# Kernel optimization log

Hardware: AMD Instinct MI355X
Metric: run time of the kernel (lower is better)

Reference implementation:

```python
import jax, jax.numpy as jnp
import numpy as np

F = 16      # frames
NV = 4096   # visual points per frame
NT = 512    # tactile points per frame
M = 4096    # model points
SCALE = 0.1


def setup_inputs() -> dict:
    key = jax.random.key(0)
    ks = jax.random.split(key, 6)
    return {
        "state": jax.random.normal(ks[0], (6,), dtype=jnp.float32) * 0.1,
        "model_points": jax.random.normal(ks[1], (M, 3), dtype=jnp.float32),
        "visual_points": jax.random.normal(ks[2], (F, NV, 3), dtype=jnp.float32),
        "tactile_points": jax.random.normal(ks[3], (F, NT, 3), dtype=jnp.float32),
        "physics_pred_states": jax.random.normal(ks[4], (F, 12), dtype=jnp.float32) * 0.1,
        "delta_time": jax.random.uniform(ks[5], (F,), dtype=jnp.float32, minval=0.01, maxval=0.05),
    }


def _skew(a):
    z = jnp.zeros((), a.dtype)
    return jnp.array([[z, -a[2], a[1]],
                      [a[2], z, -a[0]],
                      [-a[1], a[0], z]])


def _rot_from_omega(omega, dt):
    # Rodrigues: R = I + sin(theta*dt) S + (1 - cos(theta*dt)) S@S, S = skew(omega/|omega|)
    theta = jnp.linalg.norm(omega)
    ax = omega / jnp.clip(theta, 1e-8)
    S = _skew(ax)
    return jnp.eye(3, dtype=omega.dtype) + jnp.sin(theta * dt) * S + (1.0 - jnp.cos(theta * dt)) * (S @ S)


def _chamfer(pred, gt):
    # rows: pred [N,3], cols: gt [M,3]; row-min of squared distances, then mean
    d = (jnp.sum(pred * pred, axis=1)[:, None]
         + jnp.sum(gt * gt, axis=1)[None, :]
         - 2.0 * pred @ gt.T)
    return jnp.mean(jnp.min(d, axis=1))


def reference(state, model_points, visual_points, tactile_points, physics_pred_states, delta_time):
    t0 = state[:3]
    r0 = _rot_from_omega(state[3:], jnp.float32(1.0))  # Euler2Mat modeled as axis-angle

    def pose_step(carry, x):
        t, r = carry
        v, omega, dt = x
        t = t + v * dt
        r = _rot_from_omega(omega, dt) @ r
        return (t, r), (t, r)

    _, (ts, rs) = jax.lax.scan(
        pose_step, (t0, r0),
        (physics_pred_states[1:, 6:9], physics_pred_states[1:, 9:12], delta_time[1:]))
    ts = jnp.concatenate([t0[None], ts], axis=0)  # [F,3]
    rs = jnp.concatenate([r0[None], rs], axis=0)  # [F,3,3]

    def frame_loss(acc, x):
        t, r, vp, tp = x
        vc = ((vp - t) @ r) / SCALE
        tc = ((tp - t) @ r) / SCALE
        acc = acc + _chamfer(vc, model_points) + 0.1 * _chamfer(tc, model_points)
        return acc, None

    E_cd, _ = jax.lax.scan(frame_loss, jnp.zeros((), jnp.float32),
                           (ts, rs, visual_points, tactile_points))
    return E_cd
```

## Files before the change

### kernel.cpp

```cpp
#include <hip/hip_runtime.h>
#include <math.h>

#define F_    16
#define NV_   4096
#define NT_   512
#define M_    4096
#define PPF_  (NV_ + NT_)
#define NPTS_ (F_ * PPF_)
#define SCALE_INV 10.0f

#define TPB   256
#define PTSB  72
#define NBLK  (NPTS_ / PTSB)
#define NG    64
#define MPG   (M_ / NG)
#define CHM   16
#define NCH   (MPG / CHM)
#define FG    68
#define PPL   18
#define NPR   9

typedef float v2f __attribute__((ext_vector_type(2)));

__device__ inline void rot_from_omega(float ox, float oy, float oz, float dt,
                                      float* R) {
    float theta = sqrtf(ox * ox + oy * oy + oz * oz);
    float inv = 1.0f / fmaxf(theta, 1e-8f);
    float ax = ox * inv, ay = oy * inv, az = oz * inv;
    float s = sinf(theta * dt);
    float c = 1.0f - cosf(theta * dt);
    R[0] = 1.0f - c * (ay * ay + az * az);
    R[1] = -s * az + c * ax * ay;
    R[2] =  s * ay + c * ax * az;
    R[3] =  s * az + c * ax * ay;
    R[4] = 1.0f - c * (ax * ax + az * az);
    R[5] = -s * ax + c * ay * az;
    R[6] = -s * ay + c * ax * az;
    R[7] =  s * ax + c * ay * az;
    R[8] = 1.0f - c * (ax * ax + ay * ay);
}

__device__ __forceinline__ void dist6(v2f qa01, v2f qa23, v2f qb01, v2f qb23,
                                      v2f c0a, v2f c0b, v2f c0c,
                                      v2f c1a, v2f c1b, v2f c1c,
                                      v2f c2a, v2f c2b, v2f c2c, float* dmp) {
    v2f A0, A1, A2, B0, B1, B2;
    asm("v_pk_fma_f32 %0, %7, %16, %7 op_sel:[0,0,1] op_sel_hi:[0,1,1]\n\t"
        "v_pk_fma_f32 %1, %7, %17, %7 op_sel:[0,0,1] op_sel_hi:[0,1,1]\n\t"
        "v_pk_fma_f32 %2, %7, %18, %7 op_sel:[0,0,1] op_sel_hi:[0,1,1]\n\t"
        "v_pk_fma_f32 %3, %9, %16, %9 op_sel:[0,0,1] op_sel_hi:[0,1,1]\n\t"
        "v_pk_fma_f32 %4, %9, %17, %9 op_sel:[0,0,1] op_sel_hi:[0,1,1]\n\t"
        "v_pk_fma_f32 %5, %9, %18, %9 op_sel:[0,0,1] op_sel_hi:[0,1,1]\n\t"
        "v_pk_fma_f32 %0, %6, %13, %0 op_sel:[1,0,0] op_sel_hi:[1,1,1]\n\t"
        "v_pk_fma_f32 %1, %6, %14, %1 op_sel:[1,0,0] op_sel_hi:[1,1,1]\n\t"
        "v_pk_fma_f32 %2, %6, %15, %2 op_sel:[1,0,0] op_sel_hi:[1,1,1]\n\t"
        "v_pk_fma_f32 %3, %8, %13, %3 op_sel:[1,0,0] op_sel_hi:[1,1,1]\n\t"
        "v_pk_fma_f32 %4, %8, %14, %4 op_sel:[1,0,0] op_sel_hi:[1,1,1]\n\t"
        "v_pk_fma_f32 %5, %8, %15, %5 op_sel:[1,0,0] op_sel_hi:[1,1,1]\n\t"
        "v_pk_fma_f32 %0, %6, %10, %0 op_sel:[0,0,0] op_sel_hi:[0,1,1]\n\t"
        "v_pk_fma_f32 %1, %6, %11, %1 op_sel:[0,0,0] op_sel_hi:[0,1,1]\n\t"
        "v_pk_fma_f32 %2, %6, %12, %2 op_sel:[0,0,0] op_sel_hi:[0,1,1]\n\t"
        "v_pk_fma_f32 %3, %8, %10, %3 op_sel:[0,0,0] op_sel_hi:[0,1,1]\n\t"
        "v_pk_fma_f32 %4, %8, %11, %4 op_sel:[0,0,0] op_sel_hi:[0,1,1]\n\t"
        "v_pk_fma_f32 %5, %8, %12, %5 op_sel:[0,0,0] op_sel_hi:[0,1,1]"
        : "=&v"(A0), "=&v"(A1), "=&v"(A2), "=&v"(B0), "=&v"(B1), "=&v"(B2)
        : "v"(qa01), "v"(qa23), "v"(qb01), "v"(qb23),
          "v"(c0a), "v"(c0b), "v"(c0c),
          "v"(c1a), "v"(c1b), "v"(c1c),
          "v"(c2a), "v"(c2b), "v"(c2c));
    dmp[0] = fminf(fminf(A0.x, B0.x), dmp[0]);
    dmp[1] = fminf(fminf(A0.y, B0.y), dmp[1]);
    dmp[2] = fminf(fminf(A1.x, B1.x), dmp[2]);
    dmp[3] = fminf(fminf(A1.y, B1.y), dmp[3]);
    dmp[4] = fminf(fminf(A2.x, B2.x), dmp[4]);
    dmp[5] = fminf(fminf(A2.y, B2.y), dmp[5]);
}

__global__ void prep_kernel(const float* __restrict__ state,
                            const float* __restrict__ phys,
                            const float* __restrict__ dts,
                            const float* __restrict__ model,
                            float* __restrict__ ws_pose,
                            float4* __restrict__ ws_feat) {
    const int b = blockIdx.x, t = threadIdx.x;
    if (b == 0) {
        __shared__ float sRs[F_ * 9];
        __shared__ float sdt[F_ * 3];
        if (t < F_) {
            float ox, oy, oz, dt;
            if (t == 0) { ox = state[3]; oy = state[4]; oz = state[5]; dt = 1.0f; }
            else        { ox = phys[t * 12 + 9]; oy = phys[t * 12 + 10];
                          oz = phys[t * 12 + 11]; dt = dts[t]; }
            float Rs[9];
            rot_from_omega(ox, oy, oz, dt, Rs);
            for (int j = 0; j < 9; ++j) sRs[t * 9 + j] = Rs[j];
            if (t > 0) {
                sdt[t * 3 + 0] = phys[t * 12 + 6] * dt;
                sdt[t * 3 + 1] = phys[t * 12 + 7] * dt;
                sdt[t * 3 + 2] = phys[t * 12 + 8] * dt;
            }
        }
        if (t == 0) {
            float R[9];
            for (int j = 0; j < 9; ++j) R[j] = sRs[j];
            float tr[3] = {state[0], state[1], state[2]};
            for (int i = 0; i < F_; ++i) {
                if (i > 0) {
                    tr[0] += sdt[i * 3 + 0];
                    tr[1] += sdt[i * 3 + 1];
                    tr[2] += sdt[i * 3 + 2];
                    float Rn[9];
                    const float* Rsp = sRs + i * 9;
                    for (int r = 0; r < 3; ++r)
                        for (int c2 = 0; c2 < 3; ++c2)
                            Rn[r * 3 + c2] = Rsp[r * 3 + 0] * R[0 + c2] +
                                             Rsp[r * 3 + 1] * R[3 + c2] +
                                             Rsp[r * 3 + 2] * R[6 + c2];
                    for (int j = 0; j < 9; ++j) R[j] = Rn[j];
                }
                float* o = ws_pose + i * 12;
                o[0] = tr[0]; o[1] = tr[1]; o[2] = tr[2];
                for (int j = 0; j < 9; ++j) o[3 + j] = R[j] * SCALE_INV;
            }
        }
    } else {
        const int id = (b - 1) * 256 + t;
        float gx = model[id * 3 + 0], gy = model[id * 3 + 1], gz = model[id * 3 + 2];
        const int c = (id >> 4) & 3, g = id >> 6, m = id & 15;
        ws_feat[c * 1024 + g * 16 + m] =
            make_float4(-2.0f * gx, -2.0f * gy, -2.0f * gz,
                        gx * gx + gy * gy + gz * gz);
    }
}

__global__ __launch_bounds__(TPB, 4) void chamfer_main(
    const float* __restrict__ vis, const float* __restrict__ tac,
    const float* __restrict__ ws_pose, const float4* __restrict__ ws_feat,
    float* __restrict__ out) {
    __shared__ float4 feat[CHM * FG];
    __shared__ float  sdm2[NG * 80];
    __shared__ float  spose[F_ * 12];
    __shared__ float  sw[4];

    const int t  = threadIdx.x;
    const int g  = t >> 2;
    const int pl = t & 3;
    const int f  = blockIdx.x >> 6;
    const int lbase = (blockIdx.x & 63) * PTSB;

    if (t < F_ * 12) spose[t] = ws_pose[t];
#pragma unroll
    for (int j = 0; j < 4; ++j) {
        int flat = t + 256 * j;
        feat[(flat & 15) * FG + (flat >> 4)] = ws_feat[flat];
    }
    __syncthreads();

    float Rr[9], trx, try_, trz;
    {
        const float* ps = spose + f * 12;
        trx = ps[0]; try_ = ps[1]; trz = ps[2];
        for (int j = 0; j < 9; ++j) Rr[j] = ps[3 + j];
    }

    v2f c0p[NPR], c1p[NPR], c2p[NPR];
    float cn[PPL], dm[PPL];
#pragma unroll
    for (int k = 0; k < PPL; ++k) {
        int loc = lbase + pl * PPL + k;
        const float* p = (loc < NV_) ? (vis + ((size_t)f * NV_ + loc) * 3)
                                     : (tac + ((size_t)f * NT_ + (loc - NV_)) * 3);
        float d0 = p[0] - trx, d1 = p[1] - try_, d2 = p[2] - trz;
        float x = d0 * Rr[0] + d1 * Rr[3] + d2 * Rr[6];
        float y = d0 * Rr[1] + d1 * Rr[4] + d2 * Rr[7];
        float z = d0 * Rr[2] + d1 * Rr[5] + d2 * Rr[8];
        cn[k] = x * x + y * y + z * z;
        dm[k] = 3.4e38f;
        if (k & 1) { c0p[k >> 1].y = x; c1p[k >> 1].y = y; c2p[k >> 1].y = z; }
        else       { c0p[k >> 1].x = x; c1p[k >> 1].x = y; c2p[k >> 1].x = z; }
    }

    for (int c = 0;; ++c) {
#pragma unroll 2
        for (int m = 0; m < CHM; m += 2) {
            float4 ga = feat[m * FG + g];
            float4 gb = feat[(m + 1) * FG + g];
            v2f qa01 = (v2f){ga.x, ga.y}, qa23 = (v2f){ga.z, ga.w};
            v2f qb01 = (v2f){gb.x, gb.y}, qb23 = (v2f){gb.z, gb.w};
            dist6(qa01, qa23, qb01, qb23, c0p[0], c0p[1], c0p[2],
                  c1p[0], c1p[1], c1p[2], c2p[0], c2p[1], c2p[2], dm);
            dist6(qa01, qa23, qb01, qb23, c0p[3], c0p[4], c0p[5],
                  c1p[3], c1p[4], c1p[5], c2p[3], c2p[4], c2p[5], dm + 6);
            dist6(qa01, qa23, qb01, qb23, c0p[6], c0p[7], c0p[8],
                  c1p[6], c1p[7], c1p[8], c2p[6], c2p[7], c2p[8], dm + 12);
        }
        if (c == NCH - 1) break;
        __syncthreads();
#pragma unroll
        for (int j = 0; j < 4; ++j) {
            int flat = t + 256 * j;
            feat[(flat & 15) * FG + (flat >> 4)] = ws_feat[(c + 1) * 1024 + flat];
        }
        __syncthreads();
    }

    {
        float* seg = &sdm2[g * 80 + pl * 20];
#pragma unroll
        for (int k = 0; k < PPL; ++k) seg[k] = dm[k] + cn[k];
    }
    __syncthreads();

    float v = 0.0f;
    if (t < PTSB) {
        const int off = t + 2 * (t / 18);
        float mn = sdm2[off];
#pragma unroll 8
        for (int i = 1; i < NG; ++i) mn = fminf(mn, sdm2[i * 80 + off]);
        const int loc = lbase + t;
        const float w = (loc < NV_) ? (1.0f / NV_) : (0.1f / NT_);
        v = mn * w;
    }
#pragma unroll
    for (int off2 = 32; off2 > 0; off2 >>= 1) v += __shfl_down(v, off2);
    if ((t & 63) == 0) sw[t >> 6] = v;
    __syncthreads();
    if (t == 0) atomicAdd(out, sw[0] + sw[1] + sw[2] + sw[3]);
}

__global__ __launch_bounds__(TPB) void chamfer_fb(
    const float* __restrict__ state, const float* __restrict__ model,
    const float* __restrict__ vis, const float* __restrict__ tac,
    const float* __restrict__ phys, const float* __restrict__ dts,
    float* __restrict__ out) {
    __shared__ float sw[4];
    const int pt = blockIdx.x * TPB + threadIdx.x;
    const int f = pt / PPF_, loc = pt - f * PPF_;
    float R[9], tr[3] = {state[0], state[1], state[2]};
    rot_from_omega(state[3], state[4], state[5], 1.0f, R);
    for (int i = 1; i <= f; ++i) {
        float dt = dts[i];
        tr[0] += phys[i * 12 + 6] * dt;
        tr[1] += phys[i * 12 + 7] * dt;
        tr[2] += phys[i * 12 + 8] * dt;
        float Rs[9], Rn[9];
        rot_from_omega(phys[i * 12 + 9], phys[i * 12 + 10], phys[i * 12 + 11], dt, Rs);
        for (int r = 0; r < 3; ++r)
            for (int c2 = 0; c2 < 3; ++c2)
                Rn[r * 3 + c2] = Rs[r * 3 + 0] * R[0 + c2] +
                                 Rs[r * 3 + 1] * R[3 + c2] +
                                 Rs[r * 3 + 2] * R[6 + c2];
        for (int j = 0; j < 9; ++j) R[j] = Rn[j];
    }
    for (int j = 0; j < 9; ++j) R[j] *= SCALE_INV;
    const float* p = (loc < NV_) ? (vis + ((size_t)f * NV_ + loc) * 3)
                                 : (tac + ((size_t)f * NT_ + (loc - NV_)) * 3);
    float d0 = p[0] - tr[0], d1 = p[1] - tr[1], d2 = p[2] - tr[2];
    float x = d0 * R[0] + d1 * R[3] + d2 * R[6];
    float y = d0 * R[1] + d1 * R[4] + d2 * R[7];
    float z = d0 * R[2] + d1 * R[5] + d2 * R[8];
    float cn = x * x + y * y + z * z;
    float mn = 3.4e38f;
    for (int i = 0; i < M_; ++i) {
        float gx = model[i * 3], gy = model[i * 3 + 1], gz = model[i * 3 + 2];
        float gn = gx * gx + gy * gy + gz * gz;
        float dd = fmaf(-2.0f * gx, x, fmaf(-2.0f * gy, y, fmaf(-2.0f * gz, z, gn)));
        mn = fminf(mn, dd);
    }
    float w = (loc < NV_) ? (1.0f / NV_) : (0.1f / NT_);
    float v = (mn + cn) * w;
    for (int off = 32; off > 0; off >>= 1) v += __shfl_down(v, off);
    if ((threadIdx.x & 63) == 0) sw[threadIdx.x >> 6] = v;
    __syncthreads();
    if (threadIdx.x == 0) atomicAdd(out, sw[0] + sw[1] + sw[2] + sw[3]);
}

extern "C" void kernel_launch(void* const* d_in, const int* in_sizes, int n_in,
                              void* d_out, int out_size, void* d_ws, size_t ws_size,
                              hipStream_t stream) {
    const float* state = (const float*)d_in[0];
    const float* model = (const float*)d_in[1];
    const float* vis   = (const float*)d_in[2];
    const float* tac   = (const float*)d_in[3];
    const float* phys  = (const float*)d_in[4];
    const float* dts   = (const float*)d_in[5];
    float* out = (float*)d_out;

    const size_t NEED = 1024 + (size_t)M_ * sizeof(float4);
    hipMemsetAsync(out, 0, sizeof(float), stream);
    if (ws_size >= NEED) {
        float*  ws_pose = (float*)d_ws;
        float4* ws_feat = (float4*)((char*)d_ws + 1024);
        prep_kernel<<<17, 256, 0, stream>>>(state, phys, dts, model, ws_pose, ws_feat);
        chamfer_main<<<NBLK, TPB, 0, stream>>>(vis, tac, ws_pose, ws_feat, out);
    } else {
        chamfer_fb<<<NPTS_ / TPB, TPB, 0, stream>>>(state, model, vis, tac, phys,
                                                    dts, out);
    }
}
```

Before: 101.5 us.

## Split model points across grid, read features via scalar loads, add reduce kernel

Chamfer work is split over a 2D grid: each block handles 2048 points against one 128-point chunk of the model. Model features now come from uniform global loads into scalar registers instead of shared memory, which removes the LDS staging and block barriers. Per-chunk minima go to a large workspace buffer, and a separate kernel reduces them and accumulates the weighted sum. The cost is about 9.4 MB of extra global traffic, an extra launch, and a larger workspace; if the workspace is too small, the slow fallback path runs instead.

Result: slower. 107.4 us (+5.8%).

```diff
diff --git a/kernel.cpp b/kernel.cpp
--- a/kernel.cpp
+++ b/kernel.cpp
@@ -9,16 +9,13 @@
 #define NPTS_ (F_ * PPF_)
 #define SCALE_INV 10.0f
 
-#define TPB   256
-#define PTSB  72
-#define NBLK  (NPTS_ / PTSB)
-#define NG    64
-#define MPG   (M_ / NG)
-#define CHM   16
-#define NCH   (MPG / CHM)
-#define FG    68
-#define PPL   18
-#define NPR   9
+#define TPB    256
+#define NPB    36
+#define NCHUNK 32
+#define CPM    128
+#define PPT    8
+
+#define PART_OFF (72 * 1024)
 
 typedef float v2f __attribute__((ext_vector_type(2)));
 
@@ -40,40 +37,49 @@
     R[8] = 1.0f - c * (ax * ax + ay * ay);
 }
 
-__device__ __forceinline__ void dist6(v2f qa01, v2f qa23, v2f qb01, v2f qb23,
-                                      v2f c0a, v2f c0b, v2f c0c,
-                                      v2f c1a, v2f c1b, v2f c1c,
-                                      v2f c2a, v2f c2b, v2f c2c, float* dmp) {
-    v2f A0, A1, A2, B0, B1, B2;
-    asm("v_pk_fma_f32 %0, %7, %16, %7 op_sel:[0,0,1] op_sel_hi:[0,1,1]\n\t"
-        "v_pk_fma_f32 %1, %7, %17, %7 op_sel:[0,0,1] op_sel_hi:[0,1,1]\n\t"
-        "v_pk_fma_f32 %2, %7, %18, %7 op_sel:[0,0,1] op_sel_hi:[0,1,1]\n\t"
-        "v_pk_fma_f32 %3, %9, %16, %9 op_sel:[0,0,1] op_sel_hi:[0,1,1]\n\t"
-        "v_pk_fma_f32 %4, %9, %17, %9 op_sel:[0,0,1] op_sel_hi:[0,1,1]\n\t"
-        "v_pk_fma_f32 %5, %9, %18, %9 op_sel:[0,0,1] op_sel_hi:[0,1,1]\n\t"
-        "v_pk_fma_f32 %0, %6, %13, %0 op_sel:[1,0,0] op_sel_hi:[1,1,1]\n\t"
-        "v_pk_fma_f32 %1, %6, %14, %1 op_sel:[1,0,0] op_sel_hi:[1,1,1]\n\t"
-        "v_pk_fma_f32 %2, %6, %15, %2 op_sel:[1,0,0] op_sel_hi:[1,1,1]\n\t"
-        "v_pk_fma_f32 %3, %8, %13, %3 op_sel:[1,0,0] op_sel_hi:[1,1,1]\n\t"
-        "v_pk_fma_f32 %4, %8, %14, %4 op_sel:[1,0,0] op_sel_hi:[1,1,1]\n\t"
-        "v_pk_fma_f32 %5, %8, %15, %5 op_sel:[1,0,0] op_sel_hi:[1,1,1]\n\t"
-        "v_pk_fma_f32 %0, %6, %10, %0 op_sel:[0,0,0] op_sel_hi:[0,1,1]\n\t"
-        "v_pk_fma_f32 %1, %6, %11, %1 op_sel:[0,0,0] op_sel_hi:[0,1,1]\n\t"
-        "v_pk_fma_f32 %2, %6, %12, %2 op_sel:[0,0,0] op_sel_hi:[0,1,1]\n\t"
-        "v_pk_fma_f32 %3, %8, %10, %3 op_sel:[0,0,0] op_sel_hi:[0,1,1]\n\t"
-        "v_pk_fma_f32 %4, %8, %11, %4 op_sel:[0,0,0] op_sel_hi:[0,1,1]\n\t"
-        "v_pk_fma_f32 %5, %8, %12, %5 op_sel:[0,0,0] op_sel_hi:[0,1,1]"
-        : "=&v"(A0), "=&v"(A1), "=&v"(A2), "=&v"(B0), "=&v"(B1), "=&v"(B2)
-        : "v"(qa01), "v"(qa23), "v"(qb01), "v"(qb23),
-          "v"(c0a), "v"(c0b), "v"(c0c),
-          "v"(c1a), "v"(c1b), "v"(c1c),
-          "v"(c2a), "v"(c2b), "v"(c2c));
-    dmp[0] = fminf(fminf(A0.x, B0.x), dmp[0]);
-    dmp[1] = fminf(fminf(A0.y, B0.y), dmp[1]);
-    dmp[2] = fminf(fminf(A1.x, B1.x), dmp[2]);
-    dmp[3] = fminf(fminf(A1.y, B1.y), dmp[3]);
-    dmp[4] = fminf(fminf(A2.x, B2.x), dmp[4]);
-    dmp[5] = fminf(fminf(A2.y, B2.y), dmp[5]);
+__device__ __forceinline__ void pkdist2(v2f qa01, v2f qa23, v2f qb01, v2f qb23,
+                                        const v2f* c0, const v2f* c1,
+                                        const v2f* c2, float* dm) {
+    v2f A0, A1, A2, A3, B0, B1, B2, B3;
+    asm(
+        "v_pk_fma_f32 %0, %9, %20, %9  op_sel:[0,0,1] op_sel_hi:[0,1,1]\n\t"
+        "v_pk_fma_f32 %1, %9, %21, %9  op_sel:[0,0,1] op_sel_hi:[0,1,1]\n\t"
+        "v_pk_fma_f32 %2, %9, %22, %9  op_sel:[0,0,1] op_sel_hi:[0,1,1]\n\t"
+        "v_pk_fma_f32 %3, %9, %23, %9  op_sel:[0,0,1] op_sel_hi:[0,1,1]\n\t"
+        "v_pk_fma_f32 %4, %11, %20, %11 op_sel:[0,0,1] op_sel_hi:[0,1,1]\n\t"
+        "v_pk_fma_f32 %5, %11, %21, %11 op_sel:[0,0,1] op_sel_hi:[0,1,1]\n\t"
+        "v_pk_fma_f32 %6, %11, %22, %11 op_sel:[0,0,1] op_sel_hi:[0,1,1]\n\t"
+        "v_pk_fma_f32 %7, %11, %23, %11 op_sel:[0,0,1] op_sel_hi:[0,1,1]\n\t"
+        "v_pk_fma_f32 %0, %8, %16, %0  op_sel:[1,0,0] op_sel_hi:[1,1,1]\n\t"
+        "v_pk_fma_f32 %1, %8, %17, %1  op_sel:[1,0,0] op_sel_hi:[1,1,1]\n\t"
+        "v_pk_fma_f32 %2, %8, %18, %2  op_sel:[1,0,0] op_sel_hi:[1,1,1]\n\t"
+        "v_pk_fma_f32 %3, %8, %19, %3  op_sel:[1,0,0] op_sel_hi:[1,1,1]\n\t"
+        "v_pk_fma_f32 %4, %10, %16, %4 op_sel:[1,0,0] op_sel_hi:[1,1,1]\n\t"
+        "v_pk_fma_f32 %5, %10, %17, %5 op_sel:[1,0,0] op_sel_hi:[1,1,1]\n\t"
+        "v_pk_fma_f32 %6, %10, %18, %6 op_sel:[1,0,0] op_sel_hi:[1,1,1]\n\t"
+        "v_pk_fma_f32 %7, %10, %19, %7 op_sel:[1,0,0] op_sel_hi:[1,1,1]\n\t"
+        "v_pk_fma_f32 %0, %8, %12, %0  op_sel:[0,0,0] op_sel_hi:[0,1,1]\n\t"
+        "v_pk_fma_f32 %1, %8, %13, %1  op_sel:[0,0,0] op_sel_hi:[0,1,1]\n\t"
+        "v_pk_fma_f32 %2, %8, %14, %2  op_sel:[0,0,0] op_sel_hi:[0,1,1]\n\t"
+        "v_pk_fma_f32 %3, %8, %15, %3  op_sel:[0,0,0] op_sel_hi:[0,1,1]\n\t"
+        "v_pk_fma_f32 %4, %10, %12, %4 op_sel:[0,0,0] op_sel_hi:[0,1,1]\n\t"
+        "v_pk_fma_f32 %5, %10, %13, %5 op_sel:[0,0,0] op_sel_hi:[0,1,1]\n\t"
+        "v_pk_fma_f32 %6, %10, %14, %6 op_sel:[0,0,0] op_sel_hi:[0,1,1]\n\t"
+        "v_pk_fma_f32 %7, %10, %15, %7 op_sel:[0,0,0] op_sel_hi:[0,1,1]"
+        : "=&v"(A0), "=&v"(A1), "=&v"(A2), "=&v"(A3),
+          "=&v"(B0), "=&v"(B1), "=&v"(B2), "=&v"(B3)
+        : "s"(qa01), "s"(qa23), "s"(qb01), "s"(qb23),
+          "v"(c0[0]), "v"(c0[1]), "v"(c0[2]), "v"(c0[3]),
+          "v"(c1[0]), "v"(c1[1]), "v"(c1[2]), "v"(c1[3]),
+          "v"(c2[0]), "v"(c2[1]), "v"(c2[2]), "v"(c2[3]));
+    dm[0] = fminf(fminf(A0.x, B0.x), dm[0]);
+    dm[1] = fminf(fminf(A0.y, B0.y), dm[1]);
+    dm[2] = fminf(fminf(A1.x, B1.x), dm[2]);
+    dm[3] = fminf(fminf(A1.y, B1.y), dm[3]);
+    dm[4] = fminf(fminf(A2.x, B2.x), dm[4]);
+    dm[5] = fminf(fminf(A2.y, B2.y), dm[5]);
+    dm[6] = fminf(fminf(A3.x, B3.x), dm[6]);
+    dm[7] = fminf(fminf(A3.y, B3.y), dm[7]);
 }
 
 __global__ void prep_kernel(const float* __restrict__ state,
@@ -126,106 +132,78 @@
     } else {
         const int id = (b - 1) * 256 + t;
         float gx = model[id * 3 + 0], gy = model[id * 3 + 1], gz = model[id * 3 + 2];
-        const int c = (id >> 4) & 3, g = id >> 6, m = id & 15;
-        ws_feat[c * 1024 + g * 16 + m] =
-            make_float4(-2.0f * gx, -2.0f * gy, -2.0f * gz,
-                        gx * gx + gy * gy + gz * gz);
+        ws_feat[id] = make_float4(-2.0f * gx, -2.0f * gy, -2.0f * gz,
+                                  gx * gx + gy * gy + gz * gz);
     }
 }
 
 __global__ __launch_bounds__(TPB, 4) void chamfer_main(
     const float* __restrict__ vis, const float* __restrict__ tac,
     const float* __restrict__ ws_pose, const float4* __restrict__ ws_feat,
-    float* __restrict__ out) {
-    __shared__ float4 feat[CHM * FG];
-    __shared__ float  sdm2[NG * 80];
-    __shared__ float  spose[F_ * 12];
-    __shared__ float  sw[4];
-
+    float* __restrict__ partials) {
+    __shared__ float spose[F_ * 12];
     const int t  = threadIdx.x;
-    const int g  = t >> 2;
-    const int pl = t & 3;
-    const int f  = blockIdx.x >> 6;
-    const int lbase = (blockIdx.x & 63) * PTSB;
+    const int pb = blockIdx.x;
+    const int ch = blockIdx.y;
 
     if (t < F_ * 12) spose[t] = ws_pose[t];
+    __syncthreads();
+
+    v2f c0p[4], c1p[4], c2p[4];
+    float cn[PPT], dm[PPT];
 #pragma unroll
-    for (int j = 0; j < 4; ++j) {
-        int flat = t + 256 * j;
-        feat[(flat & 15) * FG + (flat >> 4)] = ws_feat[flat];
-    }
-    __syncthreads();
-
-    float Rr[9], trx, try_, trz;
-    {
-        const float* ps = spose + f * 12;
-        trx = ps[0]; try_ = ps[1]; trz = ps[2];
-        for (int j = 0; j < 9; ++j) Rr[j] = ps[3 + j];
-    }
-
-    v2f c0p[NPR], c1p[NPR], c2p[NPR];
-    float cn[PPL], dm[PPL];
-#pragma unroll
-    for (int k = 0; k < PPL; ++k) {
-        int loc = lbase + pl * PPL + k;
+    for (int k = 0; k < PPT; ++k) {
+        int pt  = pb * 2048 + k * 256 + t;
+        int f   = pt / PPF_;
+        int loc = pt - f * PPF_;
         const float* p = (loc < NV_) ? (vis + ((size_t)f * NV_ + loc) * 3)
                                      : (tac + ((size_t)f * NT_ + (loc - NV_)) * 3);
-        float d0 = p[0] - trx, d1 = p[1] - try_, d2 = p[2] - trz;
-        float x = d0 * Rr[0] + d1 * Rr[3] + d2 * Rr[6];
-        float y = d0 * Rr[1] + d1 * Rr[4] + d2 * Rr[7];
-        float z = d0 * Rr[2] + d1 * Rr[5] + d2 * Rr[8];
+        const float* ps = spose + f * 12;
+        float d0 = p[0] - ps[0], d1 = p[1] - ps[1], d2 = p[2] - ps[2];
+        const float* R = ps + 3;
+        float x = d0 * R[0] + d1 * R[3] + d2 * R[6];
+        float y = d0 * R[1] + d1 * R[4] + d2 * R[7];
+        float z = d0 * R[2] + d1 * R[5] + d2 * R[8];
         cn[k] = x * x + y * y + z * z;
         dm[k] = 3.4e38f;
         if (k & 1) { c0p[k >> 1].y = x; c1p[k >> 1].y = y; c2p[k >> 1].y = z; }
         else       { c0p[k >> 1].x = x; c1p[k >> 1].x = y; c2p[k >> 1].x = z; }
     }
 
-    for (int c = 0;; ++c) {
-#pragma unroll 2
-        for (int m = 0; m < CHM; m += 2) {
-            float4 ga = feat[m * FG + g];
-            float4 gb = feat[(m + 1) * FG + g];
-            v2f qa01 = (v2f){ga.x, ga.y}, qa23 = (v2f){ga.z, ga.w};
-            v2f qb01 = (v2f){gb.x, gb.y}, qb23 = (v2f){gb.z, gb.w};
-            dist6(qa01, qa23, qb01, qb23, c0p[0], c0p[1], c0p[2],
-                  c1p[0], c1p[1], c1p[2], c2p[0], c2p[1], c2p[2], dm);
-            dist6(qa01, qa23, qb01, qb23, c0p[3], c0p[4], c0p[5],
-                  c1p[3], c1p[4], c1p[5], c2p[3], c2p[4], c2p[5], dm + 6);
-            dist6(qa01, qa23, qb01, qb23, c0p[6], c0p[7], c0p[8],
-                  c1p[6], c1p[7], c1p[8], c2p[6], c2p[7], c2p[8], dm + 12);
-        }
-        if (c == NCH - 1) break;
-        __syncthreads();
+    const v2f* fch = (const v2f*)(ws_feat + (size_t)ch * CPM);
+#pragma unroll 4
+    for (int m = 0; m < CPM; m += 2) {
+        v2f qa01 = fch[2 * m + 0];
+        v2f qa23 = fch[2 * m + 1];
+        v2f qb01 = fch[2 * m + 2];
+        v2f qb23 = fch[2 * m + 3];
+        pkdist2(qa01, qa23, qb01, qb23, c0p, c1p, c2p, dm);
+    }
+
 #pragma unroll
-        for (int j = 0; j < 4; ++j) {
-            int flat = t + 256 * j;
-            feat[(flat & 15) * FG + (flat >> 4)] = ws_feat[(c + 1) * 1024 + flat];
-        }
-        __syncthreads();
-    }
-
-    {
-        float* seg = &sdm2[g * 80 + pl * 20];
+    for (int k = 0; k < PPT; ++k)
+        partials[(size_t)ch * NPTS_ + pb * 2048 + k * 256 + t] = dm[k] + cn[k];
+}
+
+__global__ __launch_bounds__(TPB) void chamfer_reduce(
+    const float* __restrict__ partials, float* __restrict__ out) {
+    __shared__ float sw[TPB / 64];
+    const int pt = blockIdx.x * TPB + threadIdx.x;
+    float m = partials[pt];
+    for (int ch = 1; ch < NCHUNK; ++ch)
+        m = fminf(m, partials[(size_t)ch * NPTS_ + pt]);
+    const int loc = pt % PPF_;
+    const float w = (loc < NV_) ? (1.0f / NV_) : (0.1f / NT_);
+    float v = m * w;
 #pragma unroll
-        for (int k = 0; k < PPL; ++k) seg[k] = dm[k] + cn[k];
-    }
+    for (int off = 32; off > 0; off >>= 1) v += __shfl_down(v, off);
+    if ((threadIdx.x & 63) == 0) sw[threadIdx.x >> 6] = v;
     __syncthreads();
-
-    float v = 0.0f;
-    if (t < PTSB) {
-        const int off = t + 2 * (t / 18);
-        float mn = sdm2[off];
-#pragma unroll 8
-        for (int i = 1; i < NG; ++i) mn = fminf(mn, sdm2[i * 80 + off]);
-        const int loc = lbase + t;
-        const float w = (loc < NV_) ? (1.0f / NV_) : (0.1f / NT_);
-        v = mn * w;
-    }
-#pragma unroll
-    for (int off2 = 32; off2 > 0; off2 >>= 1) v += __shfl_down(v, off2);
-    if ((t & 63) == 0) sw[t >> 6] = v;
-    __syncthreads();
-    if (t == 0) atomicAdd(out, sw[0] + sw[1] + sw[2] + sw[3]);
+    if (threadIdx.x == 0) {
+        float s = 0.0f;
+        for (int i = 0; i < TPB / 64; ++i) s += sw[i];
+        atomicAdd(out, s);
+    }
 }
 
 __global__ __launch_bounds__(TPB) void chamfer_fb(
@@ -286,13 +264,16 @@
     const float* dts   = (const float*)d_in[5];
     float* out = (float*)d_out;
 
-    const size_t NEED = 1024 + (size_t)M_ * sizeof(float4);
+    const size_t NEED = PART_OFF + (size_t)NCHUNK * NPTS_ * sizeof(float);
     hipMemsetAsync(out, 0, sizeof(float), stream);
     if (ws_size >= NEED) {
-        float*  ws_pose = (float*)d_ws;
-        float4* ws_feat = (float4*)((char*)d_ws + 1024);
+        float*  ws_pose  = (float*)d_ws;
+        float4* ws_feat  = (float4*)((char*)d_ws + 1024);
+        float*  partials = (float*)((char*)d_ws + PART_OFF);
         prep_kernel<<<17, 256, 0, stream>>>(state, phys, dts, model, ws_pose, ws_feat);
-        chamfer_main<<<NBLK, TPB, 0, stream>>>(vis, tac, ws_pose, ws_feat, out);
+        dim3 grid(NPB, NCHUNK);
+        chamfer_main<<<grid, TPB, 0, stream>>>(vis, tac, ws_pose, ws_feat, partials);
+        chamfer_reduce<<<NPTS_ / TPB, TPB, 0, stream>>>(partials, out);
     } else {
         chamfer_fb<<<NPTS_ / TPB, TPB, 0, stream>>>(state, model, vis, tac, phys,
                                                     dts, out);
```
